# Kernel tuning notes

Hardware: AMD Instinct MI355X
Metric: run time of the kernel (lower is better)

Reference implementation:

```python
import jax, jax.numpy as jnp
import numpy as np

WS = 7          # window size
NH = 16         # num heads
EPS = 1e-5      # LayerNorm eps


def _rel_pos_index(ws):
    coords = np.stack(np.meshgrid(np.arange(ws), np.arange(ws), indexing='ij'))  # [2,ws,ws]
    cf = coords.reshape(2, -1)                                                   # [2,N]
    rel = (cf[:, :, None] - cf[:, None, :]).transpose(1, 2, 0)                   # [N,N,2]
    rel[:, :, 0] += ws - 1
    rel[:, :, 1] += ws - 1
    rel[:, :, 0] *= 2 * ws - 1
    return jnp.asarray(rel.sum(-1))                                              # [N,N]


def _ln(x, w, b):
    mu = jnp.mean(x, axis=-1, keepdims=True)
    var = jnp.mean(jnp.square(x - mu), axis=-1, keepdims=True)
    return (x - mu) * jax.lax.rsqrt(var + EPS) * w + b


def setup_inputs() -> dict:
    key = jax.random.key(0)
    ks = jax.random.split(key, 10)
    B, H, W, C = 32, 28, 28, 512
    N, hd, hidden = WS * WS, C // NH, 4 * C
    inp = {
        'x': jax.random.normal(ks[0], (B, H, W, C), jnp.float32),
        'q_global': jax.random.normal(ks[1], (B, 1, NH, N, hd), jnp.float32),
        'norm1_w': jnp.ones((C,), jnp.float32),
        'norm1_b': jnp.zeros((C,), jnp.float32),
        'qkv_w': jax.random.normal(ks[2], (2 * C, C), jnp.float32) * 0.02,
        'qkv_b': jnp.zeros((2 * C,), jnp.float32),
        'rel_bias_table': jax.random.normal(ks[3], ((2 * WS - 1) ** 2, NH), jnp.float32) * 0.02,
        'proj_w': jax.random.normal(ks[4], (C, C), jnp.float32) * 0.02,
        'proj_b': jnp.zeros((C,), jnp.float32),
        'norm2_w': jnp.ones((C,), jnp.float32),
        'norm2_b': jnp.zeros((C,), jnp.float32),
        'fc1_w': jax.random.normal(ks[5], (hidden, C), jnp.float32) * 0.02,
        'fc1_b': jnp.zeros((hidden,), jnp.float32),
        'fc2_w': jax.random.normal(ks[6], (C, hidden), jnp.float32) * 0.02,
        'fc2_b': jnp.zeros((C,), jnp.float32),
    }
    return inp


def reference(x, q_global, norm1_w, norm1_b, qkv_w, qkv_b, rel_bias_table,
              proj_w, proj_b, norm2_w, norm2_b, fc1_w, fc1_b, fc2_w, fc2_b):
    B, H, W, C = x.shape
    N = WS * WS
    hd = C // NH
    scale = hd ** -0.5
    nWh, nWw = H // WS, W // WS

    shortcut = x
    h = _ln(x, norm1_w, norm1_b)

    # window partition -> [B_, N, C]
    xw = h.reshape(B, nWh, WS, nWw, WS, C).transpose(0, 1, 3, 2, 4, 5)
    xw = xw.reshape(-1, N, C)
    B_ = xw.shape[0]

    # kv projection
    kv = xw @ qkv_w.T + qkv_b                              # [B_, N, 2C]
    kv = kv.reshape(B_, N, 2, NH, hd).transpose(2, 0, 3, 1, 4)
    k, v = kv[0], kv[1]                                    # [B_, NH, N, hd]

    # global query repeated across windows of each image
    B_dim = B_ // B
    q = jnp.broadcast_to(q_global, (B, B_dim, NH, N, hd)).reshape(B_, NH, N, hd)
    q = q * scale

    attn = jnp.einsum('bhnd,bhmd->bhnm', q, k)             # [B_, NH, N, N]
    rpi = _rel_pos_index(WS)                               # [N, N]
    bias = rel_bias_table[rpi]                             # [N, N, NH]
    attn = attn + bias.transpose(2, 0, 1)[None]
    attn = jax.nn.softmax(attn, axis=-1)

    out = jnp.einsum('bhnm,bhmd->bhnd', attn, v)           # [B_, NH, N, hd]
    out = out.transpose(0, 2, 1, 3).reshape(B_, N, C)
    out = out @ proj_w.T + proj_b

    # window reverse -> [B, H, W, C]
    out = out.reshape(B, nWh, nWw, WS, WS, C).transpose(0, 1, 3, 2, 4, 5)
    out = out.reshape(B, H, W, C)

    x = shortcut + out
    h2 = _ln(x, norm2_w, norm2_b)
    m = jax.nn.gelu(h2 @ fc1_w.T + fc1_b, approximate=False)
    m = m @ fc2_w.T + fc2_b
    return x + m
```

## Files before the change

kernel.cpp:

```cpp
#include <hip/hip_runtime.h>

typedef unsigned int u32;
typedef unsigned short u16;
typedef __attribute__((ext_vector_type(8))) short short8;
typedef __attribute__((ext_vector_type(4))) float f32x4;

static __device__ __forceinline__ u16 f2bf(float f) {
    u32 u = __builtin_bit_cast(u32, f);
    u32 r = (u + 0x7fffu + ((u >> 16) & 1u)) >> 16;
    return (u16)r;
}
static __device__ __forceinline__ float bf2f(u16 b) {
    return __builtin_bit_cast(float, ((u32)b) << 16);
}

static __device__ __forceinline__ void cvt_seg(const float* __restrict__ s, u16* __restrict__ d,
                                               int n4, int base, int stride) {
    for (int i = base; i < n4; i += stride) {
        float4 v = ((const float4*)s)[i];
        ushort4 p;
        p.x = f2bf(v.x); p.y = f2bf(v.y); p.z = f2bf(v.z); p.w = f2bf(v.w);
        ((ushort4*)d)[i] = p;
    }
}
__global__ void cvt4_kernel(const float* s0, u16* d0, int n0,
                            const float* s1, u16* d1, int n1,
                            const float* s2, u16* d2, int n2,
                            const float* s3, u16* d3, int n3) {
    int base = blockIdx.x * blockDim.x + threadIdx.x;
    int stride = gridDim.x * blockDim.x;
    cvt_seg(s0, d0, n0 >> 2, base, stride);
    cvt_seg(s1, d1, n1 >> 2, base, stride);
    cvt_seg(s2, d2, n2 >> 2, base, stride);
    cvt_seg(s3, d3, n3 >> 2, base, stride);
}

__global__ __launch_bounds__(64)
void ln_kernel(const float* __restrict__ x, const float* __restrict__ w,
               const float* __restrict__ b, u16* __restrict__ out) {
    int row = blockIdx.x;
    int t = threadIdx.x;
    const float4* xr = (const float4*)(x + (size_t)row * 512);
    float4 v0 = xr[t * 2], v1 = xr[t * 2 + 1];
    float s  = v0.x + v0.y + v0.z + v0.w + v1.x + v1.y + v1.z + v1.w;
    float s2 = v0.x*v0.x + v0.y*v0.y + v0.z*v0.z + v0.w*v0.w
             + v1.x*v1.x + v1.y*v1.y + v1.z*v1.z + v1.w*v1.w;
    #pragma unroll
    for (int off = 32; off >= 1; off >>= 1) {
        s  += __shfl_xor(s, off);
        s2 += __shfl_xor(s2, off);
    }
    float mu   = s * (1.f / 512.f);
    float var  = s2 * (1.f / 512.f) - mu * mu;
    float rstd = rsqrtf(var + 1e-5f);
    int c = t * 8;
    float xv[8] = {v0.x, v0.y, v0.z, v0.w, v1.x, v1.y, v1.z, v1.w};
    short8 pk;
    #pragma unroll
    for (int j = 0; j < 8; ++j) {
        float y = (xv[j] - mu) * rstd * w[c + j] + b[c + j];
        pk[j] = (short)f2bf(y);
    }
    *(short8*)(out + (size_t)row * 512 + c) = pk;
}

#define EPI_BF16 0
#define EPI_RES  1
#define EPI_GELU 2

#define STAGE(PTRS, LDSBASE, g) { \
    const int _slot = ((g) & 3) << 14; \
    _Pragma("unroll") \
    for (int _r = 0; _r < 2; ++_r) { \
        __builtin_amdgcn_global_load_lds( \
            (const __attribute__((address_space(1))) u32*)(PTRS[_r] + (size_t)(g) * 64), \
            (__attribute__((address_space(3))) u32*)(LDSBASE + _slot + (_r * 512 + wid * 64) * 16), \
            16, 0, 0); \
    } }

#define GBODY(NV, h) { \
    const int slot = ((h) & 3) << 14; \
    short8 bF[4], aF[4]; \
    _Pragma("unroll") \
    for (int ni = 0; ni < 4; ++ni) \
        bF[ni] = *(const short8*)(ldsB + slot + wc * 4096 + ni * 1024 + laneOff); \
    _Pragma("unroll") \
    for (int mi = 0; mi < 4; ++mi) \
        aF[mi] = *(const short8*)(ldsA + slot + wr * 8192 + mi * 1024 + laneOff); \
    if ((h) + 3 < NG) STAGE(pA, ldsA, (h) + 3); \
    __builtin_amdgcn_s_barrier(); \
    asm volatile("s_waitcnt lgkmcnt(0)" ::: "memory"); \
    __builtin_amdgcn_sched_barrier(0); \
    __builtin_amdgcn_s_setprio(1); \
    _Pragma("unroll") \
    for (int mi = 0; mi < 4; ++mi) \
        _Pragma("unroll") \
        for (int ni = 0; ni < 4; ++ni) \
            acc[mi][ni] = __builtin_amdgcn_mfma_f32_16x16x32_bf16(aF[mi], bF[ni], acc[mi][ni], 0, 0, 0); \
    __builtin_amdgcn_s_setprio(0); \
    __builtin_amdgcn_sched_barrier(0); \
    __builtin_amdgcn_s_barrier(); \
    short8 aG[4]; \
    _Pragma("unroll") \
    for (int mi = 0; mi < 4; ++mi) \
        aG[mi] = *(const short8*)(ldsA + slot + wr * 8192 + (mi + 4) * 1024 + laneOff); \
    if ((h) + 3 < NG) STAGE(pB, ldsB, (h) + 3); \
    __builtin_amdgcn_s_barrier(); \
    asm volatile("s_waitcnt lgkmcnt(0)" ::: "memory"); \
    __builtin_amdgcn_sched_barrier(0); \
    __builtin_amdgcn_s_setprio(1); \
    _Pragma("unroll") \
    for (int mi = 0; mi < 4; ++mi) \
        _Pragma("unroll") \
        for (int ni = 0; ni < 4; ++ni) \
            acc[mi + 4][ni] = __builtin_amdgcn_mfma_f32_16x16x32_bf16(aG[mi], bF[ni], acc[mi + 4][ni], 0, 0, 0); \
    __builtin_amdgcn_s_setprio(0); \
    __builtin_amdgcn_sched_barrier(0); \
    if ((NV) >= 8)      { asm volatile("s_waitcnt vmcnt(8)" ::: "memory"); } \
    else if ((NV) >= 4) { asm volatile("s_waitcnt vmcnt(4)" ::: "memory"); } \
    else if ((NV) >= 0) { asm volatile("s_waitcnt vmcnt(0)" ::: "memory"); } \
    __builtin_amdgcn_s_barrier(); \
    __builtin_amdgcn_sched_barrier(0); \
}

template<int EPI, int KT>
__global__ __launch_bounds__(512, 2)
void gemm256_kernel(const u16* __restrict__ A, const u16* __restrict__ W,
                    const float* __restrict__ bias, const float* resid,
                    void* out, int N) {
    constexpr int K  = KT * 64;
    constexpr int NG = KT * 2;
    __shared__ __attribute__((aligned(16))) char lds[131072];
    char* ldsA = lds;
    char* ldsB = lds + 65536;

    const int tid  = threadIdx.x;
    const int lane = tid & 63;
    const int wid  = tid >> 6;
    const int wr   = wid >> 2;
    const int wc   = wid & 3;
    const int r15  = lane & 15, q4 = lane >> 4;

    u32 nbx = gridDim.x;
    u32 bid = blockIdx.y * nbx + blockIdx.x;
    u32 nb  = nbx * gridDim.y;
    u32 tile = bid;
    if ((nb & 7u) == 0u) tile = (bid & 7u) * (nb >> 3) + (bid >> 3);
    const int tileM = (int)(tile / nbx) * 256;
    const int tileN = (int)(tile % nbx) * 256;

    const int sp = (lane & 7) ^ (lane >> 3);
    const int coladd = (sp & 3) * 8;
    const char* pA[2]; const char* pB[2];
    #pragma unroll
    for (int r = 0; r < 2; ++r) {
        int srow = 2 * (r * 64 + wid * 8 + (lane >> 3)) + (sp >> 2);
        pA[r] = (const char*)(A + (size_t)(tileM + srow) * K + coladd);
        pB[r] = (const char*)(W + (size_t)(tileN + srow) * K + coladd);
    }
    const int laneOff = ((r15 >> 1) << 7) + ((((r15 & 1) * 4 + q4) ^ (r15 >> 1)) << 4);

    f32x4 acc[8][4] = {};

    STAGE(pA, ldsA, 0); STAGE(pB, ldsB, 0);
    STAGE(pA, ldsA, 1); STAGE(pB, ldsB, 1);
    STAGE(pA, ldsA, 2); STAGE(pB, ldsB, 2);
    asm volatile("s_waitcnt vmcnt(8)" ::: "memory");
    __builtin_amdgcn_s_barrier();
    __builtin_amdgcn_sched_barrier(0);

    #pragma unroll 1
    for (int h = 0; h <= NG - 4; ++h) GBODY(8, h)
    GBODY(4, NG - 3)
    GBODY(0, NG - 2)
    GBODY(-1, NG - 1)

    #pragma unroll
    for (int mi = 0; mi < 8; ++mi) {
        #pragma unroll
        for (int ni = 0; ni < 4; ++ni) {
            int col = tileN + wc * 64 + ni * 16 + r15;
            float bv = bias[col];
            #pragma unroll
            for (int r = 0; r < 4; ++r) {
                int row = tileM + wr * 128 + mi * 16 + q4 * 4 + r;
                float v = acc[mi][ni][r] + bv;
                if (EPI == EPI_GELU) v = 0.5f * v * (1.f + erff(v * 0.70710678118654752f));
                if (EPI == EPI_RES) {
                    v += resid[(size_t)row * N + col];
                    ((float*)out)[(size_t)row * N + col] = v;
                } else {
                    ((u16*)out)[(size_t)row * N + col] = f2bf(v);
                }
            }
        }
    }
}

__global__ __launch_bounds__(64)
void attn_kernel(const u16* __restrict__ kv, const float* __restrict__ qg,
                 const float* __restrict__ bt, u16* __restrict__ ao) {
    __shared__ u16 Vt[32][72];
    __shared__ u16 P[64][72];
    const int lane = threadIdx.x;
    const int q4 = lane >> 4, r15 = lane & 15;
    const int head = blockIdx.x & 15;
    const int w = blockIdx.x >> 4;
    const int b = w >> 4, win = w & 15, wy = win >> 2, wx = win & 3;
    const int rowbase = (b * 28 + wy * 7) * 28 + wx * 7;

    short8 kF[4];
    #pragma unroll
    for (int mj = 0; mj < 4; ++mj) {
        int j = mj * 16 + r15; int jc = j < 49 ? j : 48;
        int tok = rowbase + (jc / 7) * 28 + (jc % 7);
        kF[mj] = *(const short8*)(kv + (size_t)tok * 1024 + head * 32 + q4 * 8);
    }
    short8 qF[4];
    const float* qbase = qg + ((size_t)(b * 16 + head)) * 49 * 32;
    #pragma unroll
    for (int ni = 0; ni < 4; ++ni) {
        int i = ni * 16 + r15; int ic = i < 49 ? i : 48;
        const float4* qr = (const float4*)(qbase + ic * 32 + q4 * 8);
        float4 a = qr[0], c = qr[1];
        short8 f;
        f[0] = (short)f2bf(a.x * 0.17677669529663687f);
        f[1] = (short)f2bf(a.y * 0.17677669529663687f);
        f[2] = (short)f2bf(a.z * 0.17677669529663687f);
        f[3] = (short)f2bf(a.w * 0.17677669529663687f);
        f[4] = (short)f2bf(c.x * 0.17677669529663687f);
        f[5] = (short)f2bf(c.y * 0.17677669529663687f);
        f[6] = (short)f2bf(c.z * 0.17677669529663687f);
        f[7] = (short)f2bf(c.w * 0.17677669529663687f);
        qF[ni] = f;
    }
    {
        int j = lane;
        short8 v0 = {}, v1 = {}, v2 = {}, v3 = {};
        if (j < 49) {
            int tok = rowbase + (j / 7) * 28 + (j % 7);
            const short8* vr = (const short8*)(kv + (size_t)tok * 1024 + 512 + head * 32);
            v0 = vr[0]; v1 = vr[1]; v2 = vr[2]; v3 = vr[3];
        }
        #pragma unroll
        for (int e = 0; e < 8; ++e) {
            Vt[e][j]      = (u16)v0[e];
            Vt[8 + e][j]  = (u16)v1[e];
            Vt[16 + e][j] = (u16)v2[e];
            Vt[24 + e][j] = (u16)v3[e];
        }
    }

    f32x4 s[4][4];
    __builtin_amdgcn_s_setprio(1);
    #pragma unroll
    for (int mj = 0; mj < 4; ++mj)
        #pragma unroll
        for (int ni = 0; ni < 4; ++ni)
            s[mj][ni] = __builtin_amdgcn_mfma_f32_16x16x32_bf16(kF[mj], qF[ni], (f32x4){0.f,0.f,0.f,0.f}, 0, 0, 0);
    __builtin_amdgcn_s_setprio(0);

    int tj16[4][4]; bool jok[4][4];
    #pragma unroll
    for (int mj = 0; mj < 4; ++mj)
        #pragma unroll
        for (int r = 0; r < 4; ++r) {
            int j = mj * 16 + q4 * 4 + r;
            int jc = j < 49 ? j : 48;
            tj16[mj][r] = ((jc / 7) * 13 + (jc % 7)) * 16;
            jok[mj][r] = (j < 49);
        }

    #pragma unroll
    for (int ni = 0; ni < 4; ++ni) {
        int i = ni * 16 + r15; int ic = i < 49 ? i : 48;
        const float* btbase = bt + (((ic / 7) * 13 + (ic % 7)) + 84) * 16 + head;
        float mx = -1e30f;
        #pragma unroll
        for (int mj = 0; mj < 4; ++mj)
            #pragma unroll
            for (int r = 0; r < 4; ++r) {
                float v = s[mj][ni][r] + btbase[-tj16[mj][r]];
                v = jok[mj][r] ? v : -1e30f;
                s[mj][ni][r] = v;
                mx = fmaxf(mx, v);
            }
        mx = fmaxf(mx, __shfl_xor(mx, 16));
        mx = fmaxf(mx, __shfl_xor(mx, 32));
        float l = 0.f;
        #pragma unroll
        for (int mj = 0; mj < 4; ++mj)
            #pragma unroll
            for (int r = 0; r < 4; ++r) {
                float p = __expf(s[mj][ni][r] - mx);
                s[mj][ni][r] = p;
                l += p;
            }
        l += __shfl_xor(l, 16);
        l += __shfl_xor(l, 32);
        float inv = 1.f / l;
        #pragma unroll
        for (int mj = 0; mj < 4; ++mj) {
            ushort4 pk;
            pk.x = f2bf(s[mj][ni][0] * inv);
            pk.y = f2bf(s[mj][ni][1] * inv);
            pk.z = f2bf(s[mj][ni][2] * inv);
            pk.w = f2bf(s[mj][ni][3] * inv);
            *(ushort4*)&P[i][mj * 16 + q4 * 4] = pk;
        }
    }
    __syncthreads();

    f32x4 o[4][2] = {};
    __builtin_amdgcn_s_setprio(1);
    #pragma unroll
    for (int ks = 0; ks < 2; ++ks) {
        short8 vB0 = *(const short8*)&Vt[r15][ks * 16 + q4 * 8];
        short8 vB1 = *(const short8*)&Vt[16 + r15][ks * 16 + q4 * 8];
        #pragma unroll
        for (int mi = 0; mi < 4; ++mi) {
            short8 pA = *(const short8*)&P[mi * 16 + r15][ks * 16 + q4 * 8];
            o[mi][0] = __builtin_amdgcn_mfma_f32_16x16x32_bf16(pA, vB0, o[mi][0], 0, 0, 0);
            o[mi][1] = __builtin_amdgcn_mfma_f32_16x16x32_bf16(pA, vB1, o[mi][1], 0, 0, 0);
        }
    }
    __builtin_amdgcn_s_setprio(0);

    #pragma unroll
    for (int mi = 0; mi < 4; ++mi)
        #pragma unroll
        for (int r = 0; r < 4; ++r) {
            int i = mi * 16 + q4 * 4 + r;
            if (i < 49) {
                int tok = rowbase + (i / 7) * 28 + (i % 7);
                u16* orow = ao + (size_t)tok * 512 + head * 32 + r15;
                orow[0]  = f2bf(o[mi][0][r]);
                orow[16] = f2bf(o[mi][1][r]);
            }
        }
}

extern "C" void kernel_launch(void* const* d_in, const int* in_sizes, int n_in,
                              void* d_out, int out_size, void* d_ws, size_t ws_size,
                              hipStream_t stream) {
    const float* x     = (const float*)d_in[0];
    const float* qg    = (const float*)d_in[1];
    const float* n1w   = (const float*)d_in[2];
    const float* n1b   = (const float*)d_in[3];
    const float* qkvw  = (const float*)d_in[4];
    const float* qkvb  = (const float*)d_in[5];
    const float* rbt   = (const float*)d_in[6];
    const float* projw = (const float*)d_in[7];
    const float* projb = (const float*)d_in[8];
    const float* n2w   = (const float*)d_in[9];
    const float* n2b   = (const float*)d_in[10];
    const float* fc1w  = (const float*)d_in[11];
    const float* fc1b  = (const float*)d_in[12];
    const float* fc2w  = (const float*)d_in[13];
    const float* fc2b  = (const float*)d_in[14];

    char* ws = (char*)d_ws;
    u16* wq = (u16*)(ws + 0);
    u16* wp = (u16*)(ws + 1048576);
    u16* w1 = (u16*)(ws + 1572864);
    u16* w2 = (u16*)(ws + 3670016);
    u16* h  = (u16*)(ws + 7864320);
    u16* kv = (u16*)(ws + 33554432);
    u16* ao = (u16*)(ws + 136314880);
    float* xres = (float*)d_out;

    cvt4_kernel<<<1024, 256, 0, stream>>>(qkvw, wq, 524288,
                                          projw, wp, 262144,
                                          fc1w, w1, 1048576,
                                          fc2w, w2, 1048576);

    ln_kernel<<<25088, 64, 0, stream>>>(x, n1w, n1b, h);
    gemm256_kernel<EPI_BF16, 8 ><<<dim3(4, 98), 512, 0, stream>>>(h,  wq, qkvb, nullptr, kv, 1024);
    attn_kernel<<<8192, 64, 0, stream>>>(kv, qg, rbt, ao);
    gemm256_kernel<EPI_RES,  8 ><<<dim3(2, 98), 512, 0, stream>>>(ao, wp, projb, x, xres, 512);
    ln_kernel<<<25088, 64, 0, stream>>>(xres, n2w, n2b, h);
    gemm256_kernel<EPI_GELU, 8 ><<<dim3(8, 98), 512, 0, stream>>>(h,  w1, fc1b, nullptr, kv , 2048);
    gemm256_kernel<EPI_RES,  32><<<dim3(2, 98), 512, 0, stream>>>(kv, w2, fc2b, xres, (float*)d_out, 512);
}
```

Measured before the change: 396.1 us.

## Unroll GEMM main loop by four stages, relax vmcnt waits, use fast GELU

Restructures the GEMM k-loop into half-stage phases unrolled four stages per iteration. Each phase drops one barrier and waits on vmcnt only every second stage, with a statically known tail. The XCD-aware tile remap now also covers tile counts that are not a multiple of eight. Exact erf GELU is replaced by an Abramowitz-Stegun polynomial approximation, trading a small accuracy loss for cheaper epilogue math. Removing barriers between half-phases may risk LDS races if slot reuse is not fully covered.

```diff
diff --git a/kernel.cpp b/kernel.cpp
--- a/kernel.cpp
+++ b/kernel.cpp
@@ -12,6 +12,17 @@
 }
 static __device__ __forceinline__ float bf2f(u16 b) {
     return __builtin_bit_cast(float, ((u32)b) << 16);
+}
+
+static __device__ __forceinline__ float fast_gelu(float v) {
+    float z = fabsf(v) * 0.70710678118654752f;
+    float t = __builtin_amdgcn_rcpf(1.f + 0.3275911f * z);
+    float poly = t * (0.254829592f + t * (-0.284496736f + t * (1.421413741f
+               + t * (-1.453152027f + t * 1.061405429f))));
+    float e = __expf(-z * z);
+    float erfz = 1.f - poly * e;
+    float sgn = v < 0.f ? -erfz : erfz;
+    return 0.5f * v * (1.f + sgn);
 }
 
 static __device__ __forceinline__ void cvt_seg(const float* __restrict__ s, u16* __restrict__ d,
@@ -68,7 +79,7 @@
 #define EPI_RES  1
 #define EPI_GELU 2
 
-#define STAGE(PTRS, LDSBASE, g) { \
+#define STAGEU(PTRS, LDSBASE, g) { \
     const int _slot = ((g) & 3) << 14; \
     _Pragma("unroll") \
     for (int _r = 0; _r < 2; ++_r) { \
@@ -78,16 +89,22 @@
             16, 0, 0); \
     } }
 
-#define GBODY(NV, h) { \
-    const int slot = ((h) & 3) << 14; \
-    short8 bF[4], aF[4]; \
-    _Pragma("unroll") \
-    for (int ni = 0; ni < 4; ++ni) \
-        bF[ni] = *(const short8*)(ldsB + slot + wc * 4096 + ni * 1024 + laneOff); \
-    _Pragma("unroll") \
-    for (int mi = 0; mi < 4; ++mi) \
-        aF[mi] = *(const short8*)(ldsA + slot + wr * 8192 + mi * 1024 + laneOff); \
-    if ((h) + 3 < NG) STAGE(pA, ldsA, (h) + 3); \
+#define PHASE(g, HALF, STGP, STGB, STG_G, STG_EN, NV) { \
+    const int slot = ((g) & 3) << 14; \
+    short8 aX[4]; \
+    if ((HALF) == 0) { \
+        _Pragma("unroll") \
+        for (int ni = 0; ni < 4; ++ni) \
+            bF[ni] = *(const short8*)(ldsB + slot + wc * 4096 + ni * 1024 + laneOff); \
+        _Pragma("unroll") \
+        for (int mi = 0; mi < 4; ++mi) \
+            aX[mi] = *(const short8*)(ldsA + slot + wr * 8192 + mi * 1024 + laneOff); \
+    } else { \
+        _Pragma("unroll") \
+        for (int mi = 0; mi < 4; ++mi) \
+            aX[mi] = *(const short8*)(ldsA + slot + wr * 8192 + (mi + 4) * 1024 + laneOff); \
+    } \
+    if (STG_EN) STAGEU(STGP, STGB, STG_G); \
     __builtin_amdgcn_s_barrier(); \
     asm volatile("s_waitcnt lgkmcnt(0)" ::: "memory"); \
     __builtin_amdgcn_sched_barrier(0); \
@@ -96,40 +113,21 @@
     for (int mi = 0; mi < 4; ++mi) \
         _Pragma("unroll") \
         for (int ni = 0; ni < 4; ++ni) \
-            acc[mi][ni] = __builtin_amdgcn_mfma_f32_16x16x32_bf16(aF[mi], bF[ni], acc[mi][ni], 0, 0, 0); \
+            acc[(HALF) * 4 + mi][ni] = __builtin_amdgcn_mfma_f32_16x16x32_bf16(aX[mi], bF[ni], acc[(HALF) * 4 + mi][ni], 0, 0, 0); \
     __builtin_amdgcn_s_setprio(0); \
     __builtin_amdgcn_sched_barrier(0); \
-    __builtin_amdgcn_s_barrier(); \
-    short8 aG[4]; \
-    _Pragma("unroll") \
-    for (int mi = 0; mi < 4; ++mi) \
-        aG[mi] = *(const short8*)(ldsA + slot + wr * 8192 + (mi + 4) * 1024 + laneOff); \
-    if ((h) + 3 < NG) STAGE(pB, ldsB, (h) + 3); \
-    __builtin_amdgcn_s_barrier(); \
-    asm volatile("s_waitcnt lgkmcnt(0)" ::: "memory"); \
-    __builtin_amdgcn_sched_barrier(0); \
-    __builtin_amdgcn_s_setprio(1); \
-    _Pragma("unroll") \
-    for (int mi = 0; mi < 4; ++mi) \
-        _Pragma("unroll") \
-        for (int ni = 0; ni < 4; ++ni) \
-            acc[mi + 4][ni] = __builtin_amdgcn_mfma_f32_16x16x32_bf16(aG[mi], bF[ni], acc[mi + 4][ni], 0, 0, 0); \
-    __builtin_amdgcn_s_setprio(0); \
-    __builtin_amdgcn_sched_barrier(0); \
-    if ((NV) >= 8)      { asm volatile("s_waitcnt vmcnt(8)" ::: "memory"); } \
-    else if ((NV) >= 4) { asm volatile("s_waitcnt vmcnt(4)" ::: "memory"); } \
-    else if ((NV) >= 0) { asm volatile("s_waitcnt vmcnt(0)" ::: "memory"); } \
+    if ((NV) == 4)      { asm volatile("s_waitcnt vmcnt(4)" ::: "memory"); } \
+    else if ((NV) == 0) { asm volatile("s_waitcnt vmcnt(0)" ::: "memory"); } \
     __builtin_amdgcn_s_barrier(); \
     __builtin_amdgcn_sched_barrier(0); \
 }
 
-template<int EPI, int KT>
+template<int EPI, int NI>
 __global__ __launch_bounds__(512, 2)
 void gemm256_kernel(const u16* __restrict__ A, const u16* __restrict__ W,
                     const float* __restrict__ bias, const float* resid,
                     void* out, int N) {
-    constexpr int K  = KT * 64;
-    constexpr int NG = KT * 2;
+    constexpr int K  = NI * 128;
     __shared__ __attribute__((aligned(16))) char lds[131072];
     char* ldsA = lds;
     char* ldsB = lds + 65536;
@@ -144,8 +142,9 @@
     u32 nbx = gridDim.x;
     u32 bid = blockIdx.y * nbx + blockIdx.x;
     u32 nb  = nbx * gridDim.y;
-    u32 tile = bid;
-    if ((nb & 7u) == 0u) tile = (bid & 7u) * (nb >> 3) + (bid >> 3);
+    u32 qq = nb >> 3, rr = nb & 7;
+    u32 xcd = bid & 7, idx = bid >> 3;
+    u32 tile = (xcd < rr ? xcd * (qq + 1) : rr * (qq + 1) + (xcd - rr) * qq) + idx;
     const int tileM = (int)(tile / nbx) * 256;
     const int tileN = (int)(tile % nbx) * 256;
 
@@ -161,19 +160,38 @@
     const int laneOff = ((r15 >> 1) << 7) + ((((r15 & 1) * 4 + q4) ^ (r15 >> 1)) << 4);
 
     f32x4 acc[8][4] = {};
-
-    STAGE(pA, ldsA, 0); STAGE(pB, ldsB, 0);
-    STAGE(pA, ldsA, 1); STAGE(pB, ldsB, 1);
-    STAGE(pA, ldsA, 2); STAGE(pB, ldsB, 2);
-    asm volatile("s_waitcnt vmcnt(8)" ::: "memory");
+    short8 bF[4];
+
+    STAGEU(pA, ldsA, 0); STAGEU(pB, ldsB, 0);
+    STAGEU(pA, ldsA, 1); STAGEU(pB, ldsB, 1);
+    STAGEU(pA, ldsA, 2); STAGEU(pB, ldsB, 2);
+    asm volatile("s_waitcnt vmcnt(4)" ::: "memory");
     __builtin_amdgcn_s_barrier();
     __builtin_amdgcn_sched_barrier(0);
 
     #pragma unroll 1
-    for (int h = 0; h <= NG - 4; ++h) GBODY(8, h)
-    GBODY(4, NG - 3)
-    GBODY(0, NG - 2)
-    GBODY(-1, NG - 1)
+    for (int h = 0; h < NI - 1; ++h) {
+        const int G = h * 4;
+        PHASE(G + 0, 0, pA, ldsA, G + 3, 1, -1)
+        PHASE(G + 0, 1, pB, ldsB, G + 3, 1, -1)
+        PHASE(G + 1, 0, pA, ldsA, G + 4, 1, -1)
+        PHASE(G + 1, 1, pB, ldsB, G + 4, 1, 4)
+        PHASE(G + 2, 0, pA, ldsA, G + 5, 1, -1)
+        PHASE(G + 2, 1, pB, ldsB, G + 5, 1, -1)
+        PHASE(G + 3, 0, pA, ldsA, G + 6, 1, -1)
+        PHASE(G + 3, 1, pB, ldsB, G + 6, 1, 4)
+    }
+    {
+        const int G = (NI - 1) * 4;
+        PHASE(G + 0, 0, pA, ldsA, G + 3, 1, -1)
+        PHASE(G + 0, 1, pB, ldsB, G + 3, 1, -1)
+        PHASE(G + 1, 0, pA, ldsA, 0, 0, -1)
+        PHASE(G + 1, 1, pB, ldsB, 0, 0, 0)
+        PHASE(G + 2, 0, pA, ldsA, 0, 0, -1)
+        PHASE(G + 2, 1, pB, ldsB, 0, 0, -1)
+        PHASE(G + 3, 0, pA, ldsA, 0, 0, -1)
+        PHASE(G + 3, 1, pB, ldsB, 0, 0, -1)
+    }
 
     #pragma unroll
     for (int mi = 0; mi < 8; ++mi) {
@@ -185,7 +203,7 @@
             for (int r = 0; r < 4; ++r) {
                 int row = tileM + wr * 128 + mi * 16 + q4 * 4 + r;
                 float v = acc[mi][ni][r] + bv;
-                if (EPI == EPI_GELU) v = 0.5f * v * (1.f + erff(v * 0.70710678118654752f));
+                if (EPI == EPI_GELU) v = fast_gelu(v);
                 if (EPI == EPI_RES) {
                     v += resid[(size_t)row * N + col];
                     ((float*)out)[(size_t)row * N + col] = v;
@@ -375,10 +393,10 @@
                                           fc2w, w2, 1048576);
 
     ln_kernel<<<25088, 64, 0, stream>>>(x, n1w, n1b, h);
-    gemm256_kernel<EPI_BF16, 8 ><<<dim3(4, 98), 512, 0, stream>>>(h,  wq, qkvb, nullptr, kv, 1024);
+    gemm256_kernel<EPI_BF16, 4 ><<<dim3(4, 98), 512, 0, stream>>>(h,  wq, qkvb, nullptr, kv, 1024);
     attn_kernel<<<8192, 64, 0, stream>>>(kv, qg, rbt, ao);
-    gemm256_kernel<EPI_RES,  8 ><<<dim3(2, 98), 512, 0, stream>>>(ao, wp, projb, x, xres, 512);
+    gemm256_kernel<EPI_RES,  4 ><<<dim3(2, 98), 512, 0, stream>>>(ao, wp, projb, x, xres, 512);
     ln_kernel<<<25088, 64, 0, stream>>>(xres, n2w, n2b, h);
-    gemm256_kernel<EPI_GELU, 8 ><<<dim3(8, 98), 512, 0, stream>>>(h,  w1, fc1b, nullptr, kv , 2048);
-    gemm256_kernel<EPI_RES,  32><<<dim3(2, 98), 512, 0, stream>>>(kv, w2, fc2b, xres, (float*)d_out, 512);
-}
+    gemm256_kernel<EPI_GELU, 4 ><<<dim3(8, 98), 512, 0, stream>>>(h,  w1, fc1b, nullptr, kv , 2048);
+    gemm256_kernel<EPI_RES,  16><<<dim3(2, 98), 512, 0, stream>>>(kv, w2, fc2b, xres, (float*)d_out, 512);
+}
```

Result: faster. 379.3 us (-4.2%).
